# Performance work log

Measured on AMD Instinct MI355X. Metric: run time of the kernel, lower is better.

Reference implementation:

```python
import jax, jax.numpy as jnp
import numpy as np

B, N, K, NUM_CLASSES = 8, 4096, 16, 40
M = B * N


def _safe_norm(v):
    s = jnp.sum(v * v, axis=-1)
    return jnp.where(s > 0, jnp.sqrt(jnp.where(s > 0, s, 1.0)), 0.0)


def _angle(v1, v2):
    cn = _safe_norm(jnp.cross(v1, v2))
    d = jnp.sum(v1 * v2, axis=-1)
    ok = (cn > 0) | (d != 0)
    return jnp.where(ok, jnp.arctan2(cn, jnp.where(ok, d, 1.0)), 0.0)


def _ppf(pos_i, pos_j, n_i, n_j):
    # PyG point_pair_features: pseudo = pos_j - pos_i (j = source, i = target)
    pseudo = pos_j - pos_i
    return jnp.stack([_safe_norm(pseudo), _angle(n_i, pseudo),
                      _angle(n_j, pseudo), _angle(n_i, n_j)], axis=-1)


def _knn_edges(pos):
    # knn_graph(k=K, loop=False), per-graph; returns (src, dst) with self-loops
    # appended (PPFConv add_self_loops=True default).
    p = pos.reshape(B, N, 3)
    sq = jnp.sum(p * p, axis=-1)                                   # [B,N]
    d2 = sq[:, :, None] + sq[:, None, :] - 2.0 * jnp.einsum('bnd,bmd->bnm', p, p)
    d2 = jnp.where(jnp.eye(N, dtype=bool)[None], jnp.inf, d2)      # no loops
    _, nbr = jax.lax.top_k(-d2, K)                                  # [B,N,K]
    offs = (jnp.arange(B) * N)[:, None, None]
    src = (nbr + offs).reshape(-1)                                  # neighbors j
    dst = jnp.repeat(jnp.arange(M), K)                              # targets i
    loops = jnp.arange(M)
    return jnp.concatenate([src, loops]), jnp.concatenate([dst, loops])


def _mlp(e, w1, b1, w2, b2):
    return jax.nn.relu(e @ w1 + b1) @ w2 + b2


def setup_inputs() -> dict:
    key = jax.random.key(0)
    ks = jax.random.split(key, 12)
    pos = jax.random.normal(ks[0], (M, 3), jnp.float32)
    nrm = jax.random.normal(ks[1], (M, 3), jnp.float32)
    nrm = nrm / jnp.linalg.norm(nrm, axis=-1, keepdims=True)
    batch = jnp.repeat(jnp.arange(B, dtype=jnp.int32), N)
    s = 0.1
    return {
        'pos': pos, 'normal': nrm, 'batch': batch,
        'w1a': jax.random.normal(ks[2], (4, 32)) * s,  'b1a': jnp.zeros(32),
        'w1b': jax.random.normal(ks[3], (32, 32)) * s, 'b1b': jnp.zeros(32),
        'w2a': jax.random.normal(ks[4], (36, 32)) * s, 'b2a': jnp.zeros(32),
        'w2b': jax.random.normal(ks[5], (32, 32)) * s, 'b2b': jnp.zeros(32),
        'wc':  jax.random.normal(ks[6], (32, NUM_CLASSES)) * s,
        'bc':  jnp.zeros(NUM_CLASSES),
    }


def reference(pos, normal, batch, w1a, b1a, w1b, b1b, w2a, b2a, w2b, b2b, wc, bc):
    src, dst = _knn_edges(pos)
    feats = _ppf(pos[dst], pos[src], normal[dst], normal[src])      # [E,4]
    # conv1: x=None -> message = mlp1(ppf), scatter-max per target node
    msg1 = _mlp(feats, w1a, b1a, w1b, b1b)
    x = jax.nn.relu(jax.ops.segment_max(msg1, dst, num_segments=M))  # [M,32]
    # conv2: message = mlp2([x_j, ppf])
    msg2 = _mlp(jnp.concatenate([x[src], feats], axis=-1), w2a, b2a, w2b, b2b)
    x = jax.nn.relu(jax.ops.segment_max(msg2, dst, num_segments=M))
    # global_max_pool over each graph (uniform batch: reshape)
    g = x.reshape(B, N, 32).max(axis=1)                              # [B,32]
    return g @ wc + bc                                               # [B,40]
```

## Files before the change

### kernel.cpp

```cpp
#include <hip/hip_runtime.h>
#include <hip/hip_bf16.h>
#include <math.h>

#define NB 8
#define NN 4096
#define KK 16
#define MM (NB*NN)
#define CH 32
#define SLOTS 17
#define NCLS 40
#define BIG 3.0e38f
#define CAP 96
#define NPB 32
#define NBLK (MM/NPB)
#define BPG (NBLK/NB)
#define HROW 36
#define HALF 2048

#define OW1A 0
#define OB1A 128
#define OW1B 160
#define OB1B 1184
#define OW2A 1216
#define OB2A 2368
#define OW2B 2400
#define OB2B 3424
#define OWC  3456
#define OBC  4736
#define NWTS 4776

typedef short short8 __attribute__((ext_vector_type(8)));
typedef float f32x4  __attribute__((ext_vector_type(4)));
typedef float f32x2  __attribute__((ext_vector_type(2)));

__device__ float4 g_pos4[MM];
__device__ float4 g_nrm4[MM];
__device__ int    g_nbr[MM*KK];
__device__ float  g_u[MM*CH];
__device__ float  g_wts[NWTS];
__device__ int    g_gmaxi[NB*CH];
__device__ int    g_cnt[NB];
__device__ __align__(16) float4 g_fe4[MM*SLOTS];
__device__ __align__(16) unsigned short g_wfrag1[2][2][64][8];
__device__ __align__(16) unsigned short g_wfrag2[2][2][64][8];

__device__ __forceinline__ float bf(const __hip_bfloat16 x) { return __bfloat162float(x); }

__device__ __forceinline__ float ldf(const void* p, int i, bool f32) {
  return f32 ? ((const float*)p)[i] : bf(((const __hip_bfloat16*)p)[i]);
}

__device__ __forceinline__ float angf(float ax, float ay, float az,
                                      float bx, float by, float bz) {
  float cx = ay*bz - az*by;
  float cy = az*bx - ax*bz;
  float cz = ax*by - ay*bx;
  float s  = cx*cx + cy*cy + cz*cz;
  float cn = s > 0.f ? sqrtf(s) : 0.f;
  float d  = ax*bx + ay*by + az*bz;
  return (cn > 0.f || d != 0.f) ? atan2f(cn, d) : 0.f;
}

__device__ __forceinline__ void ppf4(const float4 pi, const float4 ni,
                                     const float4 pj, const float4 nj, float* f) {
  float px = pj.x - pi.x, py = pj.y - pi.y, pz = pj.z - pi.z;
  float s = px*px + py*py + pz*pz;
  f[0] = s > 0.f ? sqrtf(s) : 0.f;
  f[1] = angf(ni.x, ni.y, ni.z, px, py, pz);
  f[2] = angf(nj.x, nj.y, nj.z, px, py, pz);
  f[3] = angf(ni.x, ni.y, ni.z, nj.x, nj.y, nj.z);
}

__device__ __forceinline__ unsigned int fkey(float f) {
  unsigned int u = __float_as_uint(f);
  return (u & 0x80000000u) ? ~u : (u | 0x80000000u);
}
__device__ __forceinline__ float funkey(unsigned int k) {
  unsigned int u = (k & 0x80000000u) ? (k ^ 0x80000000u) : ~k;
  return __uint_as_float(u);
}

__device__ __forceinline__ unsigned int mbcnt64(unsigned long long m) {
  return __builtin_amdgcn_mbcnt_hi((unsigned int)(m >> 32),
         __builtin_amdgcn_mbcnt_lo((unsigned int)m, 0u));
}

__device__ __forceinline__ void bsplit(float v, unsigned short* hi, unsigned short* lo) {
  __hip_bfloat16 h = __float2bfloat16(v);
  float hf = __bfloat162float(h);
  __hip_bfloat16 l = __float2bfloat16(v - hf);
  *hi = *reinterpret_cast<unsigned short*>(&h);
  *lo = *reinterpret_cast<unsigned short*>(&l);
}

__device__ __forceinline__ void afrag(const float* row, short8* ah, short8* al) {
  float4 a = *(const float4*)row;
  float4 b = *(const float4*)(row + 4);
  unsigned short h, l;
  #pragma unroll
  for (int j = 0; j < 4; ++j) {
    bsplit((&a.x)[j], &h, &l); (*ah)[j]   = (short)h; (*al)[j]   = (short)l;
    bsplit((&b.x)[j], &h, &l); (*ah)[j+4] = (short)h; (*al)[j+4] = (short)l;
  }
}

__device__ __forceinline__ float ldwt(int i, bool f32,
    const void* w1a, const void* b1a, const void* w1b, const void* b1b,
    const void* w2a, const void* b2a, const void* w2b, const void* b2b,
    const void* wc, const void* bc) {
  if (i < OB1A) return ldf(w1a, i - OW1A, f32);
  if (i < OW1B) return ldf(b1a, i - OB1A, f32);
  if (i < OB1B) return ldf(w1b, i - OW1B, f32);
  if (i < OW2A) return ldf(b1b, i - OB1B, f32);
  if (i < OB2A) return ldf(w2a, i - OW2A, f32);
  if (i < OW2B) return ldf(b2a, i - OB2A, f32);
  if (i < OB2B) return ldf(w2b, i - OW2B, f32);
  if (i < OWC)  return ldf(b2b, i - OB2B, f32);
  if (i < OBC)  return ldf(wc,  i - OWC,  f32);
  return ldf(bc, i - OBC, f32);
}

__global__ __launch_bounds__(256) void prep_kernel(
    const void* __restrict__ pos, const void* __restrict__ nrm,
    const void* w1a, const void* b1a, const void* w1b, const void* b1b,
    const void* w2a, const void* b2a, const void* w2b, const void* b2b,
    const void* wc, const void* bc) {
  __shared__ int sflag;
  const int tid = threadIdx.x;
  const int bid = blockIdx.x;
  const int base = bid << 8;
  if (tid < 64) {
    const float* nf = (const float*)nrm;
    const __hip_bfloat16* nh = (const __hip_bfloat16*)nrm;
    int n = base + tid;
    float x = nf[3*n], y = nf[3*n+1], z = nf[3*n+2];
    float ss = x*x + y*y + z*z;
    bool okf = (ss > 0.98f && ss < 1.02f);
    float a = bf(nh[3*n]), b2 = bf(nh[3*n+1]), c2 = bf(nh[3*n+2]);
    float sb = a*a + b2*b2 + c2*c2;
    bool okb = (sb > 0.95f && sb < 1.05f);
    unsigned long long mf = __ballot(okf), mb = __ballot(okb);
    if (tid == 0) sflag = (__popcll(mf) >= __popcll(mb)) ? 1 : 0;
  }
  __syncthreads();
  const bool f32 = sflag != 0;
  {
    int i = base + tid;
    float x = ldf(pos, 3*i, f32), y = ldf(pos, 3*i+1, f32), z = ldf(pos, 3*i+2, f32);
    g_pos4[i] = make_float4(x, y, z, x*x + y*y + z*z);
    float a = ldf(nrm, 3*i, f32), bb = ldf(nrm, 3*i+1, f32), cc = ldf(nrm, 3*i+2, f32);
    g_nrm4[i] = make_float4(a, bb, cc, 0.f);
  }
  if (bid < 16) {
    int t = (bid << 8) + tid;
    int which = t >> 11;
    int r = t & 2047;
    int tt = r >> 10;  r &= 1023;
    int hl = r >> 9;   r &= 511;
    int ln = r >> 3;
    int j  = r & 7;
    int k = (ln >> 4)*8 + j;
    int c = tt*16 + (ln & 15);
    float wv = ldf(which ? w2b : w1b, k*CH + c, f32);
    unsigned short hi, lo;
    bsplit(wv, &hi, &lo);
    unsigned short v = hl ? lo : hi;
    if (which) g_wfrag2[tt][hl][ln][j] = v;
    else       g_wfrag1[tt][hl][ln][j] = v;
  } else if (bid < 35) {
    int i = ((bid - 16) << 8) + tid;
    if (i < NWTS)
      g_wts[i] = ldwt(i, f32, w1a, b1a, w1b, b1b, w2a, b2a, w2b, b2b, wc, bc);
  }
}

__global__ __launch_bounds__(512) void knn_conv1_kernel() {
  __shared__ __align__(16) union SU {
    struct {
      float sx[HALF], sy[HALF], sz[HALF];
      unsigned short ilst[NPB][CAP];
    } k;
    struct {
      float fe[NPB*SLOTS][4];
      float h1s[152*HROW];
      float wsaT[32*HROW];
      float xs[NPB][CH];
    } c;
  } u;
  __shared__ unsigned short nbrs[NPB][KK];

  const int tid  = threadIdx.x;
  const int w    = tid >> 6, lane = tid & 63;
  const int blk  = blockIdx.x;
  const int b    = blk >> 7;
  const int qb   = (blk & 127) << 5;
  const float4* bp = g_pos4 + b*NN;

  float q2x[4], q2y[4], q2z[4];
  #pragma unroll
  for (int qq = 0; qq < 4; ++qq) {
    float4 qv = bp[qb + (w << 2) + qq];
    q2x[qq] = -2.f*qv.x; q2y[qq] = -2.f*qv.y; q2z[qq] = -2.f*qv.z;
  }

  const f32x2* sx2 = (const f32x2*)u.k.sx;
  const f32x2* sy2 = (const f32x2*)u.k.sy;
  const f32x2* sz2 = (const f32x2*)u.k.sz;

  float mn[4];
  #pragma unroll
  for (int qq = 0; qq < 4; ++qq) mn[qq] = BIG;
  #pragma unroll 1
  for (int h = 0; h < 2; ++h) {
    #pragma unroll
    for (int k = 0; k < 4; ++k) {
      int idx = k*512 + tid;
      float4 o = bp[h*HALF + idx];
      u.k.sx[idx] = o.x; u.k.sy[idx] = o.y; u.k.sz[idx] = o.z;
    }
    __syncthreads();
    #pragma unroll 4
    for (int it = 0; it < 16; ++it) {
      int p = it*64 + lane;
      f32x2 ox = sx2[p], oy = sy2[p], oz = sz2[p];
      f32x2 ow = __builtin_elementwise_fma(oz, oz,
                 __builtin_elementwise_fma(oy, oy, ox*ox));
      #pragma unroll
      for (int qq = 0; qq < 4; ++qq) {
        f32x2 qx = {q2x[qq], q2x[qq]};
        f32x2 qy = {q2y[qq], q2y[qq]};
        f32x2 qz = {q2z[qq], q2z[qq]};
        f32x2 d = __builtin_elementwise_fma(qx, ox,
                  __builtin_elementwise_fma(qy, oy,
                  __builtin_elementwise_fma(qz, oz, ow)));
        mn[qq] = fminf(fminf(d[0], d[1]), mn[qq]);
      }
    }
    if (h == 0) __syncthreads();
  }

  unsigned int key[4], lo[4], hi[4];
  #pragma unroll
  for (int qq = 0; qq < 4; ++qq) { key[qq] = fkey(mn[qq]) >> 16; lo[qq] = 0u; hi[qq] = 0xFFFFu; }
  #pragma unroll 1
  for (int s = 0; s < 16; ++s) {
    #pragma unroll
    for (int qq = 0; qq < 4; ++qq) {
      unsigned int mid = (lo[qq] + hi[qq]) >> 1;
      int c = (int)__popcll(__ballot(key[qq] <= mid));
      if (c >= 17) hi[qq] = mid; else lo[qq] = mid + 1;
    }
  }
  float Tf[4];
  #pragma unroll
  for (int qq = 0; qq < 4; ++qq) {
    float T = funkey((hi[qq] << 16) | 0xFFFFu);
    Tf[qq] = T + 4e-5f + 1e-5f*fabsf(T);
  }

  unsigned int scnt[4];
  #pragma unroll
  for (int qq = 0; qq < 4; ++qq) scnt[qq] = 0u;
  #pragma unroll 1
  for (int hh = 0; hh < 2; ++hh) {
    const int h = 1 - hh;
    if (hh == 1) {
      __syncthreads();
      #pragma unroll
      for (int k = 0; k < 4; ++k) {
        int idx = k*512 + tid;
        float4 o = bp[h*HALF + idx];
        u.k.sx[idx] = o.x; u.k.sy[idx] = o.y; u.k.sz[idx] = o.z;
      }
      __syncthreads();
    }
    #pragma unroll 2
    for (int it = 0; it < 16; ++it) {
      int p = it*64 + lane;
      int gidx = h*HALF + 2*p;
      f32x2 ox = sx2[p], oy = sy2[p], oz = sz2[p];
      f32x2 ow = __builtin_elementwise_fma(oz, oz,
                 __builtin_elementwise_fma(oy, oy, ox*ox));
      #pragma unroll
      for (int qq = 0; qq < 4; ++qq) {
        f32x2 qx = {q2x[qq], q2x[qq]};
        f32x2 qy = {q2y[qq], q2y[qq]};
        f32x2 qz = {q2z[qq], q2z[qq]};
        f32x2 d = __builtin_elementwise_fma(qx, ox,
                  __builtin_elementwise_fma(qy, oy,
                  __builtin_elementwise_fma(qz, oz, ow)));
        bool h0 = d[0] <= Tf[qq];
        bool h1 = d[1] <= Tf[qq];
        unsigned long long mk0 = __ballot(h0);
        unsigned long long mk1 = __ballot(h1);
        if (mk0 | mk1) {
          unsigned int cbase = scnt[qq];
          if (h0) {
            unsigned int pos = cbase + mbcnt64(mk0);
            if (pos < CAP) u.k.ilst[(w<<2)|qq][pos] = (unsigned short)gidx;
          }
          cbase += (unsigned int)__popcll(mk0);
          if (h1) {
            unsigned int pos = cbase + mbcnt64(mk1);
            if (pos < CAP) u.k.ilst[(w<<2)|qq][pos] = (unsigned short)(gidx + 1);
          }
          scnt[qq] = cbase + (unsigned int)__popcll(mk1);
        }
      }
    }
  }

  #pragma unroll 1
  for (int qq = 0; qq < 4; ++qq) {
    const int ql = (w << 2) | qq;
    const int m = min((int)scnt[qq], CAP);
    const double mx = (double)(-0.5f*q2x[qq]);
    const double my_ = (double)(-0.5f*q2y[qq]);
    const double mz = (double)(-0.5f*q2z[qq]);
    const double sqme = (mx*mx + my_*my_) + mz*mz;
    if (m <= 64) {
      double d; int idx;
      if (lane < m) {
        int ci = u.k.ilst[ql][lane];
        float4 cv = bp[ci];
        double ox = (double)cv.x, oy = (double)cv.y, oz = (double)cv.z;
        double sqo = (ox*ox + oy*oy) + oz*oz;
        double dt  = (mx*ox + my_*oy) + mz*oz;
        d = (sqme + sqo) - 2.0*dt;
        idx = ci;
      } else { d = 1.0e300; idx = 0x7fffffff; }
      #pragma unroll
      for (int k = 2; k <= 64; k <<= 1) {
        #pragma unroll
        for (int j = k >> 1; j >= 1; j >>= 1) {
          double pd = __shfl_xor(d, j);
          int    pi = __shfl_xor(idx, j);
          bool mineLess = (d < pd) || (d == pd && idx < pi);
          bool wantMin  = (((lane & j) == 0) == ((lane & k) == 0));
          if (mineLess != wantMin) { d = pd; idx = pi; }
        }
      }
      if (lane >= 1 && lane <= KK) {
        nbrs[ql][lane-1] = (unsigned short)idx;
        g_nbr[(b*NN + qb + ql)*KK + (lane-1)] = b*NN + idx;
      }
    } else {
      for (int e = lane; e < m; e += 64) {
        int myi = u.k.ilst[ql][e];
        float4 cv = bp[myi];
        double ox = (double)cv.x, oy = (double)cv.y, oz = (double)cv.z;
        double myd = (sqme + ((ox*ox + oy*oy) + oz*oz))
                   - 2.0*((mx*ox + my_*oy) + mz*oz);
        int rank = 0;
        for (int o = 0; o < m; ++o) {
          int oi = u.k.ilst[ql][o];
          float4 ov = bp[oi];
          double px = (double)ov.x, py = (double)ov.y, pz = (double)ov.z;
          double od = (sqme + ((px*px + py*py) + pz*pz))
                    - 2.0*((mx*px + my_*py) + mz*pz);
          rank += (od < myd) || (od == myd && oi < myi);
        }
        if (rank >= 1 && rank <= KK) {
          nbrs[ql][rank-1] = (unsigned short)myi;
          g_nbr[(b*NN + qb + ql)*KK + (rank-1)] = b*NN + myi;
        }
      }
    }
  }

  const int c32 = tid & 31;
  const int quad = lane >> 4, l15 = lane & 15;
  float w1a_c[4];
  #pragma unroll
  for (int f = 0; f < 4; ++f) w1a_c[f] = g_wts[OW1A + f*CH + c32];
  const float b1a_c = g_wts[OB1A + c32];
  short8 bH0 = *(const short8*)&g_wfrag1[0][0][lane][0];
  short8 bL0 = *(const short8*)&g_wfrag1[0][1][lane][0];
  short8 bH1 = *(const short8*)&g_wfrag1[1][0][lane][0];
  short8 bL1 = *(const short8*)&g_wfrag1[1][1][lane][0];
  const float bias0 = g_wts[OB1B + l15];
  const float bias1 = g_wts[OB1B + 16 + l15];

  __syncthreads();

  for (int i2 = tid; i2 < 1024; i2 += 512) {
    int k = i2 >> 5, cc = i2 & 31;
    u.c.wsaT[cc*HROW + k] = g_wts[OW2A + i2];
  }
  const int nbb = b*NN + qb;
  for (int e = tid; e < NPB*SLOTS; e += 512) {
    int ns = e / 17, slot = e - ns*17;
    int ig = nbb + ns;
    int jg = (slot < KK) ? (b*NN + (int)nbrs[ns][slot]) : ig;
    float f[4];
    ppf4(g_pos4[ig], g_nrm4[ig], g_pos4[jg], g_nrm4[jg], f);
    float4 fv = make_float4(f[0], f[1], f[2], f[3]);
    *(float4*)u.c.fe[e] = fv;
    g_fe4[(size_t)nbb*SLOTS + e] = fv;
  }
  __syncthreads();

  #pragma unroll 1
  for (int ck = 0; ck < 4; ++ck) {
    #pragma unroll
    for (int it = 0; it < 9; ++it) {
      int idx = it*512 + tid;
      int e = idx >> 5;
      if (e < 136) {
        float4 f4 = *(const float4*)u.c.fe[ck*136 + e];
        float h = b1a_c + f4.x*w1a_c[0] + f4.y*w1a_c[1] + f4.z*w1a_c[2] + f4.w*w1a_c[3];
        u.c.h1s[e*HROW + c32] = fmaxf(h, 0.f);
      }
    }
    __syncthreads();
    {
      const int rbase = w*17;
      short8 ah0, al0, ah1, al1;
      afrag(&u.c.h1s[(rbase      + l15)*HROW + quad*8], &ah0, &al0);
      afrag(&u.c.h1s[(rbase + 16 + l15)*HROW + quad*8], &ah1, &al1);
      f32x4 a00 = {0.f,0.f,0.f,0.f}, a01 = a00, a10 = a00, a11 = a00;
      a00 = __builtin_amdgcn_mfma_f32_16x16x32_bf16(ah0, bH0, a00, 0, 0, 0);
      a00 = __builtin_amdgcn_mfma_f32_16x16x32_bf16(ah0, bL0, a00, 0, 0, 0);
      a00 = __builtin_amdgcn_mfma_f32_16x16x32_bf16(al0, bH0, a00, 0, 0, 0);
      a01 = __builtin_amdgcn_mfma_f32_16x16x32_bf16(ah0, bH1, a01, 0, 0, 0);
      a01 = __builtin_amdgcn_mfma_f32_16x16x32_bf16(ah0, bL1, a01, 0, 0, 0);
      a01 = __builtin_amdgcn_mfma_f32_16x16x32_bf16(al0, bH1, a01, 0, 0, 0);
      a10 = __builtin_amdgcn_mfma_f32_16x16x32_bf16(ah1, bH0, a10, 0, 0, 0);
      a10 = __builtin_amdgcn_mfma_f32_16x16x32_bf16(ah1, bL0, a10, 0, 0, 0);
      a10 = __builtin_amdgcn_mfma_f32_16x16x32_bf16(al1, bH0, a10, 0, 0, 0);
      a11 = __builtin_amdgcn_mfma_f32_16x16x32_bf16(ah1, bH1, a11, 0, 0, 0);
      a11 = __builtin_amdgcn_mfma_f32_16x16x32_bf16(ah1, bL1, a11, 0, 0, 0);
      a11 = __builtin_amdgcn_mfma_f32_16x16x32_bf16(al1, bH1, a11, 0, 0, 0);
      float m0 = fmaxf(fmaxf(a00[0], a00[1]), fmaxf(a00[2], a00[3]));
      float m1 = fmaxf(fmaxf(a01[0], a01[1]), fmaxf(a01[2], a01[3]));
      if (quad == 0) { m0 = fmaxf(m0, a10[0]); m1 = fmaxf(m1, a11[0]); }
      m0 = fmaxf(m0, __shfl_xor(m0, 16)); m0 = fmaxf(m0, __shfl_xor(m0, 32));
      m1 = fmaxf(m1, __shfl_xor(m1, 16)); m1 = fmaxf(m1, __shfl_xor(m1, 32));
      if (quad == 0) {
        u.c.xs[ck*8 + w][l15]      = fmaxf(m0 + bias0, 0.f);
        u.c.xs[ck*8 + w][16 + l15] = fmaxf(m1 + bias1, 0.f);
      }
    }
    __syncthreads();
  }
  #pragma unroll
  for (int it = 0; it < 2; ++it) {
    int ns = it*16 + (tid >> 5);
    float uu = 0.f;
    #pragma unroll
    for (int k4 = 0; k4 < 8; ++k4) {
      float4 x4 = *(const float4*)&u.c.xs[ns][4*k4];
      float4 w4 = *(const float4*)&u.c.wsaT[c32*HROW + 4*k4];
      uu += x4.x*w4.x + x4.y*w4.y + x4.z*w4.z + x4.w*w4.w;
    }
    g_u[(nbb + ns)*CH + c32] = uu;
  }
}

__global__ __launch_bounds__(512) void conv2_kernel(float* __restrict__ out) {
  __shared__ __align__(16) float fe[NPB*SLOTS][4];
  __shared__ int jn[NPB*SLOTS];
  __shared__ __align__(16) float h1s[152*HROW];
  __shared__ float xs[NPB][CH];
  __shared__ float gm2[CH];
  __shared__ int slast;
  const int tid = threadIdx.x;
  const int c = tid & 31;
  const int s16 = tid >> 5;
  const int lane = tid & 63, wv = tid >> 6;
  const int quad = lane >> 4, l15 = lane & 15;
  const int node0 = blockIdx.x << 5;
  const int g = blockIdx.x >> 7;
  float w2aL_c[4];
  #pragma unroll
  for (int f = 0; f < 4; ++f) w2aL_c[f] = g_wts[OW2A + (CH + f)*CH + c];
  const float b2a_c = g_wts[OB2A + c];
  short8 bH0 = *(const short8*)&g_wfrag2[0][0][lane][0];
  short8 bL0 = *(const short8*)&g_wfrag2[0][1][lane][0];
  short8 bH1 = *(const short8*)&g_wfrag2[1][0][lane][0];
  short8 bL1 = *(const short8*)&g_wfrag2[1][1][lane][0];
  const float bias0 = g_wts[OB2B + l15];
  const float bias1 = g_wts[OB2B + 16 + l15];

  for (int e = tid; e < NPB*SLOTS; e += 512) {
    int ns = e / 17, slot = e - ns*17;
    int i = node0 + ns;
    jn[e] = (slot < KK) ? g_nbr[i*KK + slot] : i;
    *(float4*)fe[e] = g_fe4[(size_t)node0*SLOTS + e];
  }
  __syncthreads();

  float upf[9];
  #pragma unroll
  for (int it = 0; it < 9; ++it) {
    int e = it*16 + s16;
    int ee = (e < 136) ? e : 135;
    upf[it] = g_u[jn[ee]*CH + c];
  }

  #pragma unroll 1
  for (int ck = 0; ck < 4; ++ck) {
    #pragma unroll
    for (int it = 0; it < 9; ++it) {
      int e = it*16 + s16;
      if (e < 136) {
        float4 f4 = *(const float4*)fe[ck*136 + e];
        float h = b2a_c + upf[it] + f4.x*w2aL_c[0] + f4.y*w2aL_c[1]
                + f4.z*w2aL_c[2] + f4.w*w2aL_c[3];
        h1s[e*HROW + c] = fmaxf(h, 0.f);
      }
    }
    __syncthreads();
    if (ck < 3) {
      #pragma unroll
      for (int it = 0; it < 9; ++it) {
        int e = it*16 + s16;
        int ee = (e < 136) ? e : 135;
        upf[it] = g_u[jn[(ck+1)*136 + ee]*CH + c];
      }
    }
    {
      const int rbase = wv*17;
      short8 ah0, al0, ah1, al1;
      afrag(&h1s[(rbase      + l15)*HROW + quad*8], &ah0, &al0);
      afrag(&h1s[(rbase + 16 + l15)*HROW + quad*8], &ah1, &al1);
      f32x4 a00 = {0.f,0.f,0.f,0.f}, a01 = a00, a10 = a00, a11 = a00;
      a00 = __builtin_amdgcn_mfma_f32_16x16x32_bf16(ah0, bH0, a00, 0, 0, 0);
      a00 = __builtin_amdgcn_mfma_f32_16x16x32_bf16(ah0, bL0, a00, 0, 0, 0);
      a00 = __builtin_amdgcn_mfma_f32_16x16x32_bf16(al0, bH0, a00, 0, 0, 0);
      a01 = __builtin_amdgcn_mfma_f32_16x16x32_bf16(ah0, bH1, a01, 0, 0, 0);
      a01 = __builtin_amdgcn_mfma_f32_16x16x32_bf16(ah0, bL1, a01, 0, 0, 0);
      a01 = __builtin_amdgcn_mfma_f32_16x16x32_bf16(al0, bH1, a01, 0, 0, 0);
      a10 = __builtin_amdgcn_mfma_f32_16x16x32_bf16(ah1, bH0, a10, 0, 0, 0);
      a10 = __builtin_amdgcn_mfma_f32_16x16x32_bf16(ah1, bL0, a10, 0, 0, 0);
      a10 = __builtin_amdgcn_mfma_f32_16x16x32_bf16(al1, bH0, a10, 0, 0, 0);
      a11 = __builtin_amdgcn_mfma_f32_16x16x32_bf16(ah1, bH1, a11, 0, 0, 0);
      a11 = __builtin_amdgcn_mfma_f32_16x16x32_bf16(ah1, bL1, a11, 0, 0, 0);
      a11 = __builtin_amdgcn_mfma_f32_16x16x32_bf16(al1, bH1, a11, 0, 0, 0);
      float m0 = fmaxf(fmaxf(a00[0], a00[1]), fmaxf(a00[2], a00[3]));
      float m1 = fmaxf(fmaxf(a01[0], a01[1]), fmaxf(a01[2], a01[3]));
      if (quad == 0) { m0 = fmaxf(m0, a10[0]); m1 = fmaxf(m1, a11[0]); }
      m0 = fmaxf(m0, __shfl_xor(m0, 16)); m0 = fmaxf(m0, __shfl_xor(m0, 32));
      m1 = fmaxf(m1, __shfl_xor(m1, 16)); m1 = fmaxf(m1, __shfl_xor(m1, 32));
      if (quad == 0) {
        xs[ck*8 + wv][l15]      = fmaxf(m0 + bias0, 0.f);
        xs[ck*8 + wv][16 + l15] = fmaxf(m1 + bias1, 0.f);
      }
    }
    __syncthreads();
  }
  if (tid < CH) {
    float m2 = xs[0][c];
    #pragma unroll
    for (int r = 1; r < NPB; ++r) m2 = fmaxf(m2, xs[r][c]);
    int old = atomicMax(&g_gmaxi[g*CH + c], __float_as_int(m2));
    asm volatile("" :: "v"(old));
  }
  if (tid == 0) {
    int rank = atomicAdd(&g_cnt[g], 1);
    slast = (rank == BPG - 1) ? 1 : 0;
  }
  __syncthreads();
  if (slast) {
    __builtin_amdgcn_fence(__ATOMIC_ACQUIRE, "agent");
    if (tid < CH) gm2[c] = __int_as_float(((volatile int*)g_gmaxi)[g*CH + c]);
    __syncthreads();
    if (tid < NCLS) {
      float s = g_wts[OBC + tid];
      #pragma unroll
      for (int f = 0; f < CH; ++f) s += gm2[f] * g_wts[OWC + f*NCLS + tid];
      out[g*NCLS + tid] = s;
    }
    if (tid < CH) atomicExch(&g_gmaxi[g*CH + tid], 0);
    if (tid == 0) atomicExch(&g_cnt[g], 0);
  }
}

extern "C" void kernel_launch(void* const* d_in, const int* in_sizes, int n_in,
                              void* d_out, int out_size, void* d_ws, size_t ws_size,
                              hipStream_t stream) {
  const void* pos = d_in[0];
  const void* nrm = d_in[1];
  const void* w1a = d_in[3];
  const void* b1a = d_in[4];
  const void* w1b = d_in[5];
  const void* b1b = d_in[6];
  const void* w2a = d_in[7];
  const void* b2a = d_in[8];
  const void* w2b = d_in[9];
  const void* b2b = d_in[10];
  const void* wc  = d_in[11];
  const void* bc  = d_in[12];

  prep_kernel<<<MM/256, 256, 0, stream>>>(pos, nrm, w1a, b1a, w1b, b1b,
                                          w2a, b2a, w2b, b2b, wc, bc);
  knn_conv1_kernel<<<NBLK, 512, 0, stream>>>();
  conv2_kernel<<<NBLK, 512, 0, stream>>>((float*)d_out);
}
```

Measured before the change: 196.9 us.

## Estimate kNN distance threshold from first half and pick it with bitonic sort

The candidate-distance threshold is now computed from per-lane minima over only the first 2048 points of the graph, instead of over all 4096. That half stays resident in LDS and is reused directly by the candidate-collection pass, which now runs halves in order 0 then 1, removing one reload and a barrier. The 16-step ballot/popcount binary search over 16-bit float keys is replaced with an in-register bitonic sort across the wavefront that picks the 17th smallest lane minimum. The threshold stays a valid upper bound but is looser, so more candidates may pass and risk exceeding the fixed candidate capacity.

```diff
diff --git a/kernel.cpp b/kernel.cpp
--- a/kernel.cpp
+++ b/kernel.cpp
@@ -69,15 +69,6 @@
   f[1] = angf(ni.x, ni.y, ni.z, px, py, pz);
   f[2] = angf(nj.x, nj.y, nj.z, px, py, pz);
   f[3] = angf(ni.x, ni.y, ni.z, nj.x, nj.y, nj.z);
-}
-
-__device__ __forceinline__ unsigned int fkey(float f) {
-  unsigned int u = __float_as_uint(f);
-  return (u & 0x80000000u) ? ~u : (u | 0x80000000u);
-}
-__device__ __forceinline__ float funkey(unsigned int k) {
-  unsigned int u = (k & 0x80000000u) ? (k ^ 0x80000000u) : ~k;
-  return __uint_as_float(u);
 }
 
 __device__ __forceinline__ unsigned int mbcnt64(unsigned long long m) {
@@ -207,69 +198,62 @@
   const f32x2* sy2 = (const f32x2*)u.k.sy;
   const f32x2* sz2 = (const f32x2*)u.k.sz;
 
+  #pragma unroll
+  for (int k = 0; k < 4; ++k) {
+    int idx = k*512 + tid;
+    float4 o = bp[idx];
+    u.k.sx[idx] = o.x; u.k.sy[idx] = o.y; u.k.sz[idx] = o.z;
+  }
+  __syncthreads();
   float mn[4];
   #pragma unroll
   for (int qq = 0; qq < 4; ++qq) mn[qq] = BIG;
+  #pragma unroll 4
+  for (int it = 0; it < 16; ++it) {
+    int p = it*64 + lane;
+    f32x2 ox = sx2[p], oy = sy2[p], oz = sz2[p];
+    f32x2 ow = __builtin_elementwise_fma(oz, oz,
+               __builtin_elementwise_fma(oy, oy, ox*ox));
+    #pragma unroll
+    for (int qq = 0; qq < 4; ++qq) {
+      f32x2 qx = {q2x[qq], q2x[qq]};
+      f32x2 qy = {q2y[qq], q2y[qq]};
+      f32x2 qz = {q2z[qq], q2z[qq]};
+      f32x2 d = __builtin_elementwise_fma(qx, ox,
+                __builtin_elementwise_fma(qy, oy,
+                __builtin_elementwise_fma(qz, oz, ow)));
+      mn[qq] = fminf(fminf(d[0], d[1]), mn[qq]);
+    }
+  }
+
+  float Tf[4];
+  #pragma unroll
+  for (int qq = 0; qq < 4; ++qq) {
+    float v = mn[qq];
+    #pragma unroll
+    for (int k = 2; k <= 64; k <<= 1) {
+      #pragma unroll
+      for (int j = k >> 1; j >= 1; j >>= 1) {
+        float pv = __shfl_xor(v, j);
+        bool takeMin = (((lane & j) == 0) == ((lane & k) == 0));
+        v = takeMin ? fminf(v, pv) : fmaxf(v, pv);
+      }
+    }
+    float T = __shfl(v, 16);
+    Tf[qq] = T + 4e-5f + 1e-5f*fabsf(T);
+  }
+
+  unsigned int scnt[4];
+  #pragma unroll
+  for (int qq = 0; qq < 4; ++qq) scnt[qq] = 0u;
   #pragma unroll 1
   for (int h = 0; h < 2; ++h) {
-    #pragma unroll
-    for (int k = 0; k < 4; ++k) {
-      int idx = k*512 + tid;
-      float4 o = bp[h*HALF + idx];
-      u.k.sx[idx] = o.x; u.k.sy[idx] = o.y; u.k.sz[idx] = o.z;
-    }
-    __syncthreads();
-    #pragma unroll 4
-    for (int it = 0; it < 16; ++it) {
-      int p = it*64 + lane;
-      f32x2 ox = sx2[p], oy = sy2[p], oz = sz2[p];
-      f32x2 ow = __builtin_elementwise_fma(oz, oz,
-                 __builtin_elementwise_fma(oy, oy, ox*ox));
-      #pragma unroll
-      for (int qq = 0; qq < 4; ++qq) {
-        f32x2 qx = {q2x[qq], q2x[qq]};
-        f32x2 qy = {q2y[qq], q2y[qq]};
-        f32x2 qz = {q2z[qq], q2z[qq]};
-        f32x2 d = __builtin_elementwise_fma(qx, ox,
-                  __builtin_elementwise_fma(qy, oy,
-                  __builtin_elementwise_fma(qz, oz, ow)));
-        mn[qq] = fminf(fminf(d[0], d[1]), mn[qq]);
-      }
-    }
-    if (h == 0) __syncthreads();
-  }
-
-  unsigned int key[4], lo[4], hi[4];
-  #pragma unroll
-  for (int qq = 0; qq < 4; ++qq) { key[qq] = fkey(mn[qq]) >> 16; lo[qq] = 0u; hi[qq] = 0xFFFFu; }
-  #pragma unroll 1
-  for (int s = 0; s < 16; ++s) {
-    #pragma unroll
-    for (int qq = 0; qq < 4; ++qq) {
-      unsigned int mid = (lo[qq] + hi[qq]) >> 1;
-      int c = (int)__popcll(__ballot(key[qq] <= mid));
-      if (c >= 17) hi[qq] = mid; else lo[qq] = mid + 1;
-    }
-  }
-  float Tf[4];
-  #pragma unroll
-  for (int qq = 0; qq < 4; ++qq) {
-    float T = funkey((hi[qq] << 16) | 0xFFFFu);
-    Tf[qq] = T + 4e-5f + 1e-5f*fabsf(T);
-  }
-
-  unsigned int scnt[4];
-  #pragma unroll
-  for (int qq = 0; qq < 4; ++qq) scnt[qq] = 0u;
-  #pragma unroll 1
-  for (int hh = 0; hh < 2; ++hh) {
-    const int h = 1 - hh;
-    if (hh == 1) {
+    if (h == 1) {
       __syncthreads();
       #pragma unroll
       for (int k = 0; k < 4; ++k) {
         int idx = k*512 + tid;
-        float4 o = bp[h*HALF + idx];
+        float4 o = bp[HALF + idx];
         u.k.sx[idx] = o.x; u.k.sy[idx] = o.y; u.k.sz[idx] = o.z;
       }
       __syncthreads();
```

After: 216.7 us. 10.1% more time.
